# Performance work log

Measured on AMD Instinct MI355X. Metric: run time of the kernel, lower is better.

The kernel has to match this reference:

```python
import jax, jax.numpy as jnp
import numpy as np

N, E, B = 50000, 600000, 64
C_IN, H, C_OUT, L = 128, 128, 64, 3
BN_EPS = 1e-5


def setup_inputs() -> dict:
    key = jax.random.key(0)
    ks = iter(jax.random.split(key, 40))

    def w(shape, fan_in):
        return jax.random.normal(next(ks), shape, jnp.float32) / np.sqrt(fan_in).astype(np.float32)

    return {
        "x": jax.random.normal(next(ks), (N, C_IN), jnp.float32),
        "edge_index": jax.random.randint(next(ks), (2, E), 0, N),
        "batch": jnp.sort(jax.random.randint(next(ks), (N,), 0, B)),
        # GINConv MLPs: Linear(in,h) -> BN -> ReLU -> Linear(h,h)   (stacked over L; C_IN == H)
        "convW1": w((L, C_IN, H), C_IN), "convb1": jnp.zeros((L, H), jnp.float32),
        "bn_g": jnp.ones((L, H), jnp.float32), "bn_b": jnp.zeros((L, H), jnp.float32),
        "convW2": w((L, H, H), H), "convb2": jnp.zeros((L, H), jnp.float32),
        # reconstruction head: Linear(h,h)-ReLU-Linear(h,h)-ReLU-Linear(h,4)-ReLU
        "recW1": w((H, H), H), "recb1": jnp.zeros((H,), jnp.float32),
        "recW2": w((H, H), H), "recb2": jnp.zeros((H,), jnp.float32),
        "recW3": w((H, 4), H), "recb3": jnp.zeros((4,), jnp.float32),
        # final MLP([h,h,out], norm=None): Linear(h,h)-ReLU-(dropout, eval=identity)-Linear(h,out)
        "mlpW1": w((H, H), H), "mlpb1": jnp.zeros((H,), jnp.float32),
        "mlpW2": w((H, C_OUT), H), "mlpb2": jnp.zeros((C_OUT,), jnp.float32),
    }


def reference(x, edge_index, batch, convW1, convb1, bn_g, bn_b, convW2, convb2,
              recW1, recb1, recW2, recb2, recW3, recb3, mlpW1, mlpb1, mlpW2, mlpb2):
    src, dst = edge_index[0], edge_index[1]
    for l in range(L):
        # GIN aggregation: out_i = nn((1+eps)*x_i + sum_{j->i} x_j), eps = 0
        agg = jax.ops.segment_sum(x[src], dst, num_segments=N)  # [N, d]
        h = (x + agg) @ convW1[l] + convb1[l]                   # [N, H]
        mu = h.mean(axis=0)
        var = jnp.var(h, axis=0)                                # biased, torch BN train mode
        h = bn_g[l] * (h - mu) * jax.lax.rsqrt(var + BN_EPS) + bn_b[l]
        h = jax.nn.relu(h) @ convW2[l] + convb2[l]
        x = jax.nn.relu(h)                                      # outer .relu() in forward
    # reconstruction branch on node features
    x_rec = jax.nn.relu(x @ recW1 + recb1)
    x_rec = jax.nn.relu(x_rec @ recW2 + recb2)
    x_rec = jax.nn.relu(x_rec @ recW3 + recb3)                  # [N, 4]
    # global_add_pool keyed by graph id
    pooled = jax.ops.segment_sum(x, batch, num_segments=B)      # [B, H]
    out = jax.nn.relu(pooled @ mlpW1 + mlpb1) @ mlpW2 + mlpb2   # [B, C_OUT]
    return (out, x_rec)
```

## Files before the change

### kernel.cpp

```cpp
#include <hip/hip_runtime.h>

#define NN 50000
#define EE 600000
#define BB 64
#define CH 128
#define LL 3
#define NGB 391
#define NSB 196
#define NPB 392

typedef unsigned short u16;
typedef unsigned int u32;
typedef short s16x8 __attribute__((ext_vector_type(8)));
typedef float f32x4 __attribute__((ext_vector_type(4)));

__device__ __forceinline__ u16 f2b(float f) {
    u32 x = __float_as_uint(f);
    return (u16)((x + 0x7FFFu + ((x >> 16) & 1u)) >> 16);
}
__device__ __forceinline__ float b2f(u16 u) {
    return __uint_as_float(((u32)u) << 16);
}

__global__ __launch_bounds__(256) void k_zero2(int* __restrict__ deg,
                                               float* __restrict__ pooled,
                                               float* __restrict__ gstats) {
    int i = blockIdx.x * 256 + threadIdx.x;
    if (i < NN) deg[i] = 0;
    int j = i - NN;
    if (j >= 0 && j < BB * CH) pooled[j] = 0.f;
    int k = j - BB * CH;
    if (k >= 0 && k < 3 * 256) gstats[k] = 0.f;
}

__global__ __launch_bounds__(256) void k_count(const int* __restrict__ ei,
                                               int* __restrict__ deg) {
    int e = blockIdx.x * 256 + threadIdx.x;
    if (e < EE) atomicAdd(&deg[ei[EE + e]], 1);
}

__global__ __launch_bounds__(256) void k_scanA(const int* __restrict__ deg,
                                               int* __restrict__ bsum) {
    __shared__ int sm[256];
    int i = blockIdx.x * 256 + threadIdx.x;
    sm[threadIdx.x] = (i < NN) ? deg[i] : 0;
    __syncthreads();
    for (int off = 128; off > 0; off >>= 1) {
        if (threadIdx.x < off) sm[threadIdx.x] += sm[threadIdx.x + off];
        __syncthreads();
    }
    if (threadIdx.x == 0) bsum[blockIdx.x] = sm[0];
}

__global__ __launch_bounds__(256) void k_scanB(const int* __restrict__ deg,
                                               const int* __restrict__ bsum,
                                               int* __restrict__ rowptr,
                                               int* __restrict__ cur) {
    __shared__ int sb[256], sd[256];
    int t = threadIdx.x;
    sb[t] = (t < NSB) ? bsum[t] : 0;
    __syncthreads();
    for (int off = 1; off < 256; off <<= 1) {
        int v = (t >= off) ? sb[t - off] : 0;
        __syncthreads();
        sb[t] += v;
        __syncthreads();
    }
    int blockOff = (blockIdx.x == 0) ? 0 : sb[blockIdx.x - 1];
    int i = blockIdx.x * 256 + t;
    int d = (i < NN) ? deg[i] : 0;
    sd[t] = d;
    __syncthreads();
    for (int off = 1; off < 256; off <<= 1) {
        int v = (t >= off) ? sd[t - off] : 0;
        __syncthreads();
        sd[t] += v;
        __syncthreads();
    }
    int excl = blockOff + sd[t] - d;
    if (i < NN) { rowptr[i] = excl; cur[i] = excl; }
    if (i == NN - 1) rowptr[NN] = excl + d;
}

__global__ __launch_bounds__(256) void k_fill(const int* __restrict__ ei,
                                              int* __restrict__ cur,
                                              int* __restrict__ perm) {
    int e = blockIdx.x * 256 + threadIdx.x;
    if (e < EE) {
        int dst = ei[EE + e];
        int idx = atomicAdd(&cur[dst], 1);
        perm[idx] = ei[e];
    }
}

__global__ __launch_bounds__(256) void k_cvt(const float* __restrict__ x,
                                             u16* __restrict__ y) {
    long base = (long)(blockIdx.x * 256 + threadIdx.x) * 8;
    if (base < (long)NN * CH) {
        float4 f0 = *(const float4*)(x + base);
        float4 f1 = *(const float4*)(x + base + 4);
        union { u16 pk[8]; uint4 v; } uu;
        uu.pk[0] = f2b(f0.x); uu.pk[1] = f2b(f0.y);
        uu.pk[2] = f2b(f0.z); uu.pk[3] = f2b(f0.w);
        uu.pk[4] = f2b(f1.x); uu.pk[5] = f2b(f1.y);
        uu.pk[6] = f2b(f1.z); uu.pk[7] = f2b(f1.w);
        *(uint4*)(y + base) = uu.v;
    }
}

__global__ __launch_bounds__(256) void k_gather(const u16* __restrict__ x,
                                                const int* __restrict__ rowptr,
                                                const int* __restrict__ perm,
                                                u16* __restrict__ y) {
    int dst = blockIdx.x * 16 + (threadIdx.x >> 4);
    if (dst >= NN) return;
    int lane = threadIdx.x & 15;
    int co = lane * 8;
    int beg = rowptr[dst], end = rowptr[dst + 1];
    union { u16 pk[8]; uint4 v; } uu;
    uu.v = *(const uint4*)(x + (long)dst * CH + co);
    float a[8], b[8];
#pragma unroll
    for (int j = 0; j < 8; ++j) { a[j] = b2f(uu.pk[j]); b[j] = 0.f; }
    int e = beg;
    for (; e + 1 < end; e += 2) {
        int s0 = perm[e], s1 = perm[e + 1];
        union { u16 pk[8]; uint4 v; } v0, v1;
        v0.v = *(const uint4*)(x + (long)s0 * CH + co);
        v1.v = *(const uint4*)(x + (long)s1 * CH + co);
#pragma unroll
        for (int j = 0; j < 8; ++j) { a[j] += b2f(v0.pk[j]); b[j] += b2f(v1.pk[j]); }
    }
    if (e < end) {
        int s0 = perm[e];
        union { u16 pk[8]; uint4 v; } v0;
        v0.v = *(const uint4*)(x + (long)s0 * CH + co);
#pragma unroll
        for (int j = 0; j < 8; ++j) a[j] += b2f(v0.pk[j]);
    }
    union { u16 pk[8]; uint4 v; } ov;
#pragma unroll
    for (int j = 0; j < 8; ++j) ov.pk[j] = f2b(a[j] + b[j]);
    *(uint4*)(y + (long)dst * CH + co) = ov.v;
}

__global__ __launch_bounds__(256) void k_transpose_all(
    const float* __restrict__ cW1, const float* __restrict__ cW2,
    const float* __restrict__ rW1, const float* __restrict__ rW2,
    const float* __restrict__ rW3, u16* __restrict__ Wt) {
    int idx = blockIdx.x * 256 + threadIdx.x;
    if (idx < 8 * 16384) {
        int slot = idx >> 14;
        int wi = idx & 16383;
        int k = wi >> 7, n = wi & 127;
        const float* src = slot < 3 ? cW1 + slot * 16384
                         : slot < 6 ? cW2 + (slot - 3) * 16384
                         : slot == 6 ? rW1 : rW2;
        Wt[slot * 16384 + n * 128 + k] = f2b(src[wi]);
    } else if (idx < 9 * 16384) {
        int j = idx - 8 * 16384;
        int n = j >> 7, k = j & 127;
        Wt[8 * 16384 + j] = (n < 4) ? f2b(rW3[k * 4 + n]) : (u16)0;
    }
}

__device__ __forceinline__ void stageB8(const u16* __restrict__ Wt, u16* sB,
                                        int s, int rr) {
#pragma unroll
    for (int it = 0; it < 8; ++it) {
        int n = it * 16 + rr;
        uint4 u = *(const uint4*)(Wt + n * CH + 8 * s);
        *(uint4*)(&sB[n * CH + ((s ^ (n & 15)) * 8)]) = u;
    }
}

__device__ __forceinline__ void mfma8(const u16* sA, const u16* sB,
                                      f32x4 acc[2][8], int wv, int quad, int l16) {
    f32x4 z = {0.f, 0.f, 0.f, 0.f};
#pragma unroll
    for (int m = 0; m < 2; ++m)
#pragma unroll
        for (int t = 0; t < 8; ++t) acc[m][t] = z;
    const u16* pa0 = sA + (wv * 32 + l16) * CH;
    const u16* pa1 = pa0 + 16 * CH;
#pragma unroll
    for (int kc = 0; kc < 4; ++kc) {
        int off = (((kc << 2) | quad) ^ l16) << 3;
        s16x8 a0 = *(const s16x8*)(pa0 + off);
        s16x8 a1 = *(const s16x8*)(pa1 + off);
#pragma unroll
        for (int t = 0; t < 8; ++t) {
            s16x8 bfr = *(const s16x8*)(sB + (t * 16 + l16) * CH + off);
            acc[0][t] = __builtin_amdgcn_mfma_f32_16x16x32_bf16(a0, bfr, acc[0][t], 0, 0, 0);
            acc[1][t] = __builtin_amdgcn_mfma_f32_16x16x32_bf16(a1, bfr, acc[1][t], 0, 0, 0);
        }
    }
}

__device__ __forceinline__ void biasrelu(f32x4 acc[2][8],
                                         const float* __restrict__ bias, int l16) {
#pragma unroll
    for (int t = 0; t < 8; ++t) {
        float bv = bias[t * 16 + l16];
#pragma unroll
        for (int m = 0; m < 2; ++m)
#pragma unroll
            for (int r = 0; r < 4; ++r)
                acc[m][t][r] = fmaxf(acc[m][t][r] + bv, 0.f);
    }
}

__device__ __forceinline__ void restage(const f32x4 acc[2][8], u16* sA,
                                        int wv, int quad, int l16) {
#pragma unroll
    for (int t = 0; t < 8; ++t) {
        int chunk = (t << 1) | (l16 >> 3);
        int o7 = l16 & 7;
#pragma unroll
        for (int m = 0; m < 2; ++m)
#pragma unroll
            for (int r = 0; r < 4; ++r) {
                int lr = wv * 32 + m * 16 + quad * 4 + r;
                sA[lr * CH + ((chunk ^ (lr & 15)) << 3) + o7] = f2b(acc[m][t][r]);
            }
    }
}

__global__ __launch_bounds__(256, 2) void k_gemm1(
    u16* __restrict__ hy, const u16* __restrict__ Wt, int layer,
    const float* __restrict__ cb1, float* __restrict__ gstats) {
    __shared__ u16 sA[128 * CH];
    __shared__ u16 sB[128 * CH];
    const int tid = threadIdx.x;
    const int s = tid & 15, rr = tid >> 4;
    const int r0 = blockIdx.x * 128;
    const int lane = tid & 63, wv = tid >> 6, quad = lane >> 4, l16 = lane & 15;

    stageB8(Wt + layer * 16384, sB, s, rr);
#pragma unroll
    for (int it = 0; it < 8; ++it) {
        int lr = it * 16 + rr, gr = r0 + lr;
        union { u16 pk[8]; uint4 v; } uu;
        if (gr < NN) {
            uu.v = *(const uint4*)(hy + (long)gr * CH + 8 * s);
        } else {
#pragma unroll
            for (int j = 0; j < 8; ++j) uu.pk[j] = 0;
        }
        *(uint4*)(&sA[lr * CH + ((s ^ (lr & 15)) * 8)]) = uu.v;
    }
    __syncthreads();
    f32x4 acc[2][8];
    mfma8(sA, sB, acc, wv, quad, l16);

    float ss[8], qq[8];
#pragma unroll
    for (int t = 0; t < 8; ++t) {
        float bv = cb1[t * 16 + l16];
        ss[t] = 0.f; qq[t] = 0.f;
#pragma unroll
        for (int m = 0; m < 2; ++m) {
            int rbase = r0 + wv * 32 + m * 16 + quad * 4;
#pragma unroll
            for (int r = 0; r < 4; ++r) {
                float v = acc[m][t][r] + bv;
                acc[m][t][r] = v;
                if (rbase + r < NN) { ss[t] += v; qq[t] += v * v; }
            }
        }
    }
#pragma unroll
    for (int t = 0; t < 8; ++t) {
        ss[t] += __shfl_xor(ss[t], 16);
        ss[t] += __shfl_xor(ss[t], 32);
        qq[t] += __shfl_xor(qq[t], 16);
        qq[t] += __shfl_xor(qq[t], 32);
    }
    float* red = (float*)sA;
    __syncthreads();
    if (lane < 16) {
#pragma unroll
        for (int t = 0; t < 8; ++t) {
            red[wv * 256 + t * 16 + l16] = ss[t];
            red[wv * 256 + 128 + t * 16 + l16] = qq[t];
        }
    }
    __syncthreads();
    unsafeAtomicAdd(&gstats[tid],
                    red[tid] + red[256 + tid] + red[512 + tid] + red[768 + tid]);

#pragma unroll
    for (int t = 0; t < 8; ++t) {
        int col = t * 16 + l16;
#pragma unroll
        for (int m = 0; m < 2; ++m)
#pragma unroll
            for (int r = 0; r < 4; ++r) {
                int row = r0 + wv * 32 + m * 16 + quad * 4 + r;
                if (row < NN) hy[(long)row * CH + col] = f2b(acc[m][t][r]);
            }
    }
}

template <bool LAST>
__global__ __launch_bounds__(256, 2) void k_gemm2(
    const u16* __restrict__ h16, const u16* __restrict__ Wt, int layer,
    const float* __restrict__ g, const float* __restrict__ bbeta,
    const float* __restrict__ gstats, const float* __restrict__ cb2,
    u16* __restrict__ xc,
    const float* __restrict__ rb1, const float* __restrict__ rb2,
    const float* __restrict__ rb3, float* __restrict__ x_rec) {
    __shared__ u16 sA[128 * CH];
    __shared__ u16 sB[128 * CH];
    __shared__ float snorm[256];
    const int tid = threadIdx.x;
    const int s = tid & 15, rr = tid >> 4;
    const int r0 = blockIdx.x * 128;
    const int lane = tid & 63, wv = tid >> 6, quad = lane >> 4, l16 = lane & 15;

    if (tid < 128) {
        float sum = gstats[tid];
        float sq = gstats[128 + tid];
        float mu = sum / (float)NN;
        float var = sq / (float)NN - mu * mu;
        float sc = g[tid] * rsqrtf(var + 1e-5f);
        snorm[tid] = sc;
        snorm[128 + tid] = bbeta[tid] - mu * sc;
    }
    stageB8(Wt + (3 + layer) * 16384, sB, s, rr);
    __syncthreads();

#pragma unroll
    for (int it = 0; it < 8; ++it) {
        int lr = it * 16 + rr, gr = r0 + lr;
        union { u16 pk[8]; uint4 v; } uu;
        if (gr < NN) {
            uu.v = *(const uint4*)(h16 + (long)gr * CH + 8 * s);
#pragma unroll
            for (int j = 0; j < 8; ++j) {
                int c = 8 * s + j;
                float v = fmaxf(b2f(uu.pk[j]) * snorm[c] + snorm[128 + c], 0.f);
                uu.pk[j] = f2b(v);
            }
        } else {
#pragma unroll
            for (int j = 0; j < 8; ++j) uu.pk[j] = 0;
        }
        *(uint4*)(&sA[lr * CH + ((s ^ (lr & 15)) * 8)]) = uu.v;
    }
    __syncthreads();
    f32x4 acc[2][8];
    mfma8(sA, sB, acc, wv, quad, l16);
    biasrelu(acc, cb2, l16);
#pragma unroll
    for (int t = 0; t < 8; ++t) {
        int col = t * 16 + l16;
#pragma unroll
        for (int m = 0; m < 2; ++m)
#pragma unroll
            for (int r = 0; r < 4; ++r) {
                int row = r0 + wv * 32 + m * 16 + quad * 4 + r;
                if (row < NN) xc[(long)row * CH + col] = f2b(acc[m][t][r]);
            }
    }

    if constexpr (LAST) {
        __syncthreads();
        restage(acc, sA, wv, quad, l16);
        stageB8(Wt + 6 * 16384, sB, s, rr);
        __syncthreads();
        mfma8(sA, sB, acc, wv, quad, l16);
        biasrelu(acc, rb1, l16);
        __syncthreads();
        restage(acc, sA, wv, quad, l16);
        stageB8(Wt + 7 * 16384, sB, s, rr);
        __syncthreads();
        mfma8(sA, sB, acc, wv, quad, l16);
        biasrelu(acc, rb2, l16);
        __syncthreads();
        restage(acc, sA, wv, quad, l16);
        {
            int n = rr;
            uint4 u = *(const uint4*)(Wt + 8 * 16384 + n * CH + 8 * s);
            *(uint4*)(&sB[n * CH + ((s ^ (n & 15)) * 8)]) = u;
        }
        __syncthreads();
        f32x4 a4[2];
        a4[0] = (f32x4){0.f, 0.f, 0.f, 0.f};
        a4[1] = (f32x4){0.f, 0.f, 0.f, 0.f};
        const u16* pa0 = sA + (wv * 32 + l16) * CH;
        const u16* pa1 = pa0 + 16 * CH;
#pragma unroll
        for (int kc = 0; kc < 4; ++kc) {
            int off = (((kc << 2) | quad) ^ l16) << 3;
            s16x8 a0 = *(const s16x8*)(pa0 + off);
            s16x8 a1 = *(const s16x8*)(pa1 + off);
            s16x8 bfr = *(const s16x8*)(sB + l16 * CH + off);
            a4[0] = __builtin_amdgcn_mfma_f32_16x16x32_bf16(a0, bfr, a4[0], 0, 0, 0);
            a4[1] = __builtin_amdgcn_mfma_f32_16x16x32_bf16(a1, bfr, a4[1], 0, 0, 0);
        }
        if (l16 < 4) {
            float bv = rb3[l16];
#pragma unroll
            for (int m = 0; m < 2; ++m)
#pragma unroll
                for (int r = 0; r < 4; ++r) {
                    int row = r0 + wv * 32 + m * 16 + quad * 4 + r;
                    if (row < NN) x_rec[(long)row * 4 + l16] = fmaxf(a4[m][r] + bv, 0.f);
                }
        }
    }
}

__global__ __launch_bounds__(256) void k_pool(const u16* __restrict__ x,
                                              const int* __restrict__ batch,
                                              float* __restrict__ pooled) {
    int r0 = blockIdx.x * 128;
    if (r0 >= NN) return;
    int rend = r0 + 128 < NN ? r0 + 128 : NN;
    int c = threadIdx.x & 127;
    int half = threadIdx.x >> 7;
    int r = r0 + half;
    if (r >= rend) return;
    int g = batch[r];
    float s = 0.f;
    for (; r < rend; r += 2) {
        int gg = batch[r];
        if (gg != g) {
            unsafeAtomicAdd(pooled + g * CH + c, s);
            s = 0.f;
            g = gg;
        }
        s += b2f(x[(long)r * CH + c]);
    }
    unsafeAtomicAdd(pooled + g * CH + c, s);
}

__global__ __launch_bounds__(128) void k_mlp(const float* __restrict__ pooled,
                                             const float* __restrict__ W1,
                                             const float* __restrict__ b1,
                                             const float* __restrict__ W2,
                                             const float* __restrict__ b2,
                                             float* __restrict__ out) {
    __shared__ float p[128], t1[128];
    int b = blockIdx.x, t = threadIdx.x;
    p[t] = pooled[b * CH + t];
    __syncthreads();
    float acc = b1[t];
    for (int k = 0; k < 128; ++k) acc += p[k] * W1[k * 128 + t];
    t1[t] = fmaxf(acc, 0.f);
    __syncthreads();
    if (t < 64) {
        float o = b2[t];
        for (int k = 0; k < 128; ++k) o += t1[k] * W2[k * 64 + t];
        out[b * 64 + t] = o;
    }
}

extern "C" void kernel_launch(void* const* d_in, const int* in_sizes, int n_in,
                              void* d_out, int out_size, void* d_ws, size_t ws_size,
                              hipStream_t stream) {
    const float* x_in   = (const float*)d_in[0];
    const int*   ei     = (const int*)d_in[1];
    const int*   batch  = (const int*)d_in[2];
    const float* convW1 = (const float*)d_in[3];
    const float* convb1 = (const float*)d_in[4];
    const float* bn_g   = (const float*)d_in[5];
    const float* bn_b   = (const float*)d_in[6];
    const float* convW2 = (const float*)d_in[7];
    const float* convb2 = (const float*)d_in[8];
    const float* recW1  = (const float*)d_in[9];
    const float* recb1  = (const float*)d_in[10];
    const float* recW2  = (const float*)d_in[11];
    const float* recb2  = (const float*)d_in[12];
    const float* recW3  = (const float*)d_in[13];
    const float* recb3  = (const float*)d_in[14];
    const float* mlpW1  = (const float*)d_in[15];
    const float* mlpb1  = (const float*)d_in[16];
    const float* mlpW2  = (const float*)d_in[17];
    const float* mlpb2  = (const float*)d_in[18];

    float* out   = (float*)d_out;
    float* x_rec = out + 4096;

    char* w = (char*)d_ws;
    u16*   x16    = (u16*)w;    w += (size_t)NN * CH * 2;
    u16*   y16    = (u16*)w;    w += (size_t)NN * CH * 2;
    u16*   xc     = (u16*)w;    w += (size_t)NN * CH * 2;
    u16*   Wt     = (u16*)w;    w += (size_t)9 * 16384 * 2;
    float* gstats = (float*)w;  w += (size_t)3 * 256 * 4;
    float* pooled = (float*)w;  w += (size_t)BB * CH * 4;
    int*   deg    = (int*)w;    w += (size_t)NN * 4;
    int*   bsum   = (int*)w;    w += (size_t)NSB * 4;
    int*   rowptr = (int*)w;    w += (size_t)(NN + 1) * 4;
    int*   cur    = (int*)w;    w += (size_t)NN * 4;
    int*   perm   = (int*)w;    w += (size_t)EE * 4;

    dim3 b256(256), b128(128);

    k_zero2<<<231, b256, 0, stream>>>(deg, pooled, gstats);
    k_count<<<2344, b256, 0, stream>>>(ei, deg);
    k_scanA<<<NSB, b256, 0, stream>>>(deg, bsum);
    k_scanB<<<NSB, b256, 0, stream>>>(deg, bsum, rowptr, cur);
    k_fill<<<2344, b256, 0, stream>>>(ei, cur, perm);
    k_cvt<<<3125, b256, 0, stream>>>(x_in, x16);
    k_transpose_all<<<576, b256, 0, stream>>>(convW1, convW2, recW1, recW2, recW3, Wt);

    const u16* cur_x = x16;
    for (int l = 0; l < LL; ++l) {
        k_gather<<<3125, b256, 0, stream>>>(cur_x, rowptr, perm, y16);
        k_gemm1<<<NGB, b256, 0, stream>>>(y16, Wt, l, convb1 + l * 128,
                                          gstats + l * 256);
        if (l < LL - 1)
            k_gemm2<false><<<NGB, b256, 0, stream>>>(
                y16, Wt, l, bn_g + l * 128, bn_b + l * 128, gstats + l * 256,
                convb2 + l * 128, xc, recb1, recb2, recb3, x_rec);
        else
            k_gemm2<true><<<NGB, b256, 0, stream>>>(
                y16, Wt, l, bn_g + l * 128, bn_b + l * 128, gstats + l * 256,
                convb2 + l * 128, xc, recb1, recb2, recb3, x_rec);
        cur_x = xc;
    }
    k_pool<<<NPB, b256, 0, stream>>>(xc, batch, pooled);
    k_mlp<<<64, b128, 0, stream>>>(pooled, mlpW1, mlpb1, mlpW2, mlpb2, out);
}
```

Before: 383.0 us.

## Fuse neighbor gather into first GEMM, shrink row tile, merge prep kernels

The CSR neighbor aggregation moves into the first GEMM kernel, so each block builds its A tile in shared memory straight from gathered rows and never writes or re-reads an intermediate aggregate buffer. The row tile drops from 128 to 64, which doubles the block count and raises occupancy to 3 blocks per CU. The conversion, weight transpose and zeroing kernels are merged into one prep launch. In exchange, the GEMM blocks now carry the irregular gather latency, and each block restages the weight tile to serve half as many rows.

```diff
diff --git a/kernel.cpp b/kernel.cpp
--- a/kernel.cpp
+++ b/kernel.cpp
@@ -5,7 +5,8 @@
 #define BB 64
 #define CH 128
 #define LL 3
-#define NGB 391
+#define TR 64
+#define NGB 782
 #define NSB 196
 #define NPB 392
 
@@ -22,15 +23,44 @@
     return __uint_as_float(((u32)u) << 16);
 }
 
-__global__ __launch_bounds__(256) void k_zero2(int* __restrict__ deg,
-                                               float* __restrict__ pooled,
-                                               float* __restrict__ gstats) {
-    int i = blockIdx.x * 256 + threadIdx.x;
-    if (i < NN) deg[i] = 0;
-    int j = i - NN;
-    if (j >= 0 && j < BB * CH) pooled[j] = 0.f;
-    int k = j - BB * CH;
-    if (k >= 0 && k < 3 * 256) gstats[k] = 0.f;
+__global__ __launch_bounds__(256) void k_prep(
+    const float* __restrict__ x, u16* __restrict__ x16,
+    const float* __restrict__ cW1, const float* __restrict__ cW2,
+    const float* __restrict__ rW1, const float* __restrict__ rW2,
+    const float* __restrict__ rW3, u16* __restrict__ Wt,
+    int* __restrict__ deg, float* __restrict__ pooled,
+    float* __restrict__ gstats) {
+    int gid = blockIdx.x * 256 + threadIdx.x;
+
+    long base = (long)gid * 8;
+    if (base < (long)NN * CH) {
+        float4 f0 = *(const float4*)(x + base);
+        float4 f1 = *(const float4*)(x + base + 4);
+        union { u16 pk[8]; uint4 v; } uu;
+        uu.pk[0] = f2b(f0.x); uu.pk[1] = f2b(f0.y);
+        uu.pk[2] = f2b(f0.z); uu.pk[3] = f2b(f0.w);
+        uu.pk[4] = f2b(f1.x); uu.pk[5] = f2b(f1.y);
+        uu.pk[6] = f2b(f1.z); uu.pk[7] = f2b(f1.w);
+        *(uint4*)(x16 + base) = uu.v;
+    }
+    if (gid < 8 * 16384) {
+        int slot = gid >> 14;
+        int wi = gid & 16383;
+        int k = wi >> 7, n = wi & 127;
+        const float* src = slot < 3 ? cW1 + slot * 16384
+                         : slot < 6 ? cW2 + (slot - 3) * 16384
+                         : slot == 6 ? rW1 : rW2;
+        Wt[slot * 16384 + n * 128 + k] = f2b(src[wi]);
+    } else if (gid < 9 * 16384) {
+        int j = gid - 8 * 16384;
+        int n = j >> 7, k = j & 127;
+        Wt[8 * 16384 + j] = (n < 4) ? f2b(rW3[k * 4 + n]) : (u16)0;
+    }
+    if (gid < NN) deg[gid] = 0;
+    int j2 = gid - NN;
+    if (j2 >= 0 && j2 < BB * CH) pooled[j2] = 0.f;
+    int k2 = j2 - BB * CH;
+    if (k2 >= 0 && k2 < 3 * 256) gstats[k2] = 0.f;
 }
 
 __global__ __launch_bounds__(256) void k_count(const int* __restrict__ ei,
@@ -93,77 +123,6 @@
     }
 }
 
-__global__ __launch_bounds__(256) void k_cvt(const float* __restrict__ x,
-                                             u16* __restrict__ y) {
-    long base = (long)(blockIdx.x * 256 + threadIdx.x) * 8;
-    if (base < (long)NN * CH) {
-        float4 f0 = *(const float4*)(x + base);
-        float4 f1 = *(const float4*)(x + base + 4);
-        union { u16 pk[8]; uint4 v; } uu;
-        uu.pk[0] = f2b(f0.x); uu.pk[1] = f2b(f0.y);
-        uu.pk[2] = f2b(f0.z); uu.pk[3] = f2b(f0.w);
-        uu.pk[4] = f2b(f1.x); uu.pk[5] = f2b(f1.y);
-        uu.pk[6] = f2b(f1.z); uu.pk[7] = f2b(f1.w);
-        *(uint4*)(y + base) = uu.v;
-    }
-}
-
-__global__ __launch_bounds__(256) void k_gather(const u16* __restrict__ x,
-                                                const int* __restrict__ rowptr,
-                                                const int* __restrict__ perm,
-                                                u16* __restrict__ y) {
-    int dst = blockIdx.x * 16 + (threadIdx.x >> 4);
-    if (dst >= NN) return;
-    int lane = threadIdx.x & 15;
-    int co = lane * 8;
-    int beg = rowptr[dst], end = rowptr[dst + 1];
-    union { u16 pk[8]; uint4 v; } uu;
-    uu.v = *(const uint4*)(x + (long)dst * CH + co);
-    float a[8], b[8];
-#pragma unroll
-    for (int j = 0; j < 8; ++j) { a[j] = b2f(uu.pk[j]); b[j] = 0.f; }
-    int e = beg;
-    for (; e + 1 < end; e += 2) {
-        int s0 = perm[e], s1 = perm[e + 1];
-        union { u16 pk[8]; uint4 v; } v0, v1;
-        v0.v = *(const uint4*)(x + (long)s0 * CH + co);
-        v1.v = *(const uint4*)(x + (long)s1 * CH + co);
-#pragma unroll
-        for (int j = 0; j < 8; ++j) { a[j] += b2f(v0.pk[j]); b[j] += b2f(v1.pk[j]); }
-    }
-    if (e < end) {
-        int s0 = perm[e];
-        union { u16 pk[8]; uint4 v; } v0;
-        v0.v = *(const uint4*)(x + (long)s0 * CH + co);
-#pragma unroll
-        for (int j = 0; j < 8; ++j) a[j] += b2f(v0.pk[j]);
-    }
-    union { u16 pk[8]; uint4 v; } ov;
-#pragma unroll
-    for (int j = 0; j < 8; ++j) ov.pk[j] = f2b(a[j] + b[j]);
-    *(uint4*)(y + (long)dst * CH + co) = ov.v;
-}
-
-__global__ __launch_bounds__(256) void k_transpose_all(
-    const float* __restrict__ cW1, const float* __restrict__ cW2,
-    const float* __restrict__ rW1, const float* __restrict__ rW2,
-    const float* __restrict__ rW3, u16* __restrict__ Wt) {
-    int idx = blockIdx.x * 256 + threadIdx.x;
-    if (idx < 8 * 16384) {
-        int slot = idx >> 14;
-        int wi = idx & 16383;
-        int k = wi >> 7, n = wi & 127;
-        const float* src = slot < 3 ? cW1 + slot * 16384
-                         : slot < 6 ? cW2 + (slot - 3) * 16384
-                         : slot == 6 ? rW1 : rW2;
-        Wt[slot * 16384 + n * 128 + k] = f2b(src[wi]);
-    } else if (idx < 9 * 16384) {
-        int j = idx - 8 * 16384;
-        int n = j >> 7, k = j & 127;
-        Wt[8 * 16384 + j] = (n < 4) ? f2b(rW3[k * 4 + n]) : (u16)0;
-    }
-}
-
 __device__ __forceinline__ void stageB8(const u16* __restrict__ Wt, u16* sB,
                                         int s, int rr) {
 #pragma unroll
@@ -174,99 +133,130 @@
     }
 }
 
-__device__ __forceinline__ void mfma8(const u16* sA, const u16* sB,
-                                      f32x4 acc[2][8], int wv, int quad, int l16) {
+template <int M>
+__device__ __forceinline__ void mfmaT(const u16* sA, const u16* sB,
+                                      f32x4 (&acc)[M][8], int rowbase, int quad,
+                                      int l16) {
     f32x4 z = {0.f, 0.f, 0.f, 0.f};
 #pragma unroll
-    for (int m = 0; m < 2; ++m)
+    for (int m = 0; m < M; ++m)
 #pragma unroll
         for (int t = 0; t < 8; ++t) acc[m][t] = z;
-    const u16* pa0 = sA + (wv * 32 + l16) * CH;
-    const u16* pa1 = pa0 + 16 * CH;
 #pragma unroll
     for (int kc = 0; kc < 4; ++kc) {
         int off = (((kc << 2) | quad) ^ l16) << 3;
-        s16x8 a0 = *(const s16x8*)(pa0 + off);
-        s16x8 a1 = *(const s16x8*)(pa1 + off);
+        s16x8 a[M];
+#pragma unroll
+        for (int m = 0; m < M; ++m)
+            a[m] = *(const s16x8*)(sA + (rowbase + m * 16 + l16) * CH + off);
 #pragma unroll
         for (int t = 0; t < 8; ++t) {
             s16x8 bfr = *(const s16x8*)(sB + (t * 16 + l16) * CH + off);
-            acc[0][t] = __builtin_amdgcn_mfma_f32_16x16x32_bf16(a0, bfr, acc[0][t], 0, 0, 0);
-            acc[1][t] = __builtin_amdgcn_mfma_f32_16x16x32_bf16(a1, bfr, acc[1][t], 0, 0, 0);
-        }
-    }
-}
-
-__device__ __forceinline__ void biasrelu(f32x4 acc[2][8],
-                                         const float* __restrict__ bias, int l16) {
+#pragma unroll
+            for (int m = 0; m < M; ++m)
+                acc[m][t] = __builtin_amdgcn_mfma_f32_16x16x32_bf16(a[m], bfr, acc[m][t], 0, 0, 0);
+        }
+    }
+}
+
+template <int M>
+__device__ __forceinline__ void biasreluT(f32x4 (&acc)[M][8],
+                                          const float* __restrict__ bias, int l16) {
 #pragma unroll
     for (int t = 0; t < 8; ++t) {
         float bv = bias[t * 16 + l16];
 #pragma unroll
-        for (int m = 0; m < 2; ++m)
+        for (int m = 0; m < M; ++m)
 #pragma unroll
             for (int r = 0; r < 4; ++r)
                 acc[m][t][r] = fmaxf(acc[m][t][r] + bv, 0.f);
     }
 }
 
-__device__ __forceinline__ void restage(const f32x4 acc[2][8], u16* sA,
-                                        int wv, int quad, int l16) {
+template <int M>
+__device__ __forceinline__ void restageT(const f32x4 (&acc)[M][8], u16* sA,
+                                         int rowbase, int quad, int l16) {
 #pragma unroll
     for (int t = 0; t < 8; ++t) {
         int chunk = (t << 1) | (l16 >> 3);
         int o7 = l16 & 7;
 #pragma unroll
-        for (int m = 0; m < 2; ++m)
+        for (int m = 0; m < M; ++m)
 #pragma unroll
             for (int r = 0; r < 4; ++r) {
-                int lr = wv * 32 + m * 16 + quad * 4 + r;
+                int lr = rowbase + m * 16 + quad * 4 + r;
                 sA[lr * CH + ((chunk ^ (lr & 15)) << 3) + o7] = f2b(acc[m][t][r]);
             }
     }
 }
 
-__global__ __launch_bounds__(256, 2) void k_gemm1(
-    u16* __restrict__ hy, const u16* __restrict__ Wt, int layer,
-    const float* __restrict__ cb1, float* __restrict__ gstats) {
-    __shared__ u16 sA[128 * CH];
+__global__ __launch_bounds__(256, 3) void k_gg1(
+    const u16* __restrict__ x, const int* __restrict__ rowptr,
+    const int* __restrict__ perm, const u16* __restrict__ Wt, int layer,
+    const float* __restrict__ cb1, float* __restrict__ gstats,
+    u16* __restrict__ h16) {
+    __shared__ u16 sA[TR * CH];
     __shared__ u16 sB[128 * CH];
     const int tid = threadIdx.x;
     const int s = tid & 15, rr = tid >> 4;
-    const int r0 = blockIdx.x * 128;
+    const int r0 = blockIdx.x * TR;
     const int lane = tid & 63, wv = tid >> 6, quad = lane >> 4, l16 = lane & 15;
 
     stageB8(Wt + layer * 16384, sB, s, rr);
-#pragma unroll
-    for (int it = 0; it < 8; ++it) {
-        int lr = it * 16 + rr, gr = r0 + lr;
-        union { u16 pk[8]; uint4 v; } uu;
-        if (gr < NN) {
-            uu.v = *(const uint4*)(hy + (long)gr * CH + 8 * s);
-        } else {
-#pragma unroll
-            for (int j = 0; j < 8; ++j) uu.pk[j] = 0;
-        }
-        *(uint4*)(&sA[lr * CH + ((s ^ (lr & 15)) * 8)]) = uu.v;
-    }
-    __syncthreads();
-    f32x4 acc[2][8];
-    mfma8(sA, sB, acc, wv, quad, l16);
+
+    {
+        int co = s * 8;
+#pragma unroll
+        for (int rl = rr; rl < TR; rl += 16) {
+            int dst = r0 + rl;
+            float a[8], b[8];
+#pragma unroll
+            for (int j = 0; j < 8; ++j) { a[j] = 0.f; b[j] = 0.f; }
+            if (dst < NN) {
+                union { u16 pk[8]; uint4 v; } uu;
+                uu.v = *(const uint4*)(x + (long)dst * CH + co);
+#pragma unroll
+                for (int j = 0; j < 8; ++j) a[j] = b2f(uu.pk[j]);
+                int beg = rowptr[dst], end = rowptr[dst + 1];
+                int e = beg;
+                for (; e + 1 < end; e += 2) {
+                    int s0 = perm[e], s1 = perm[e + 1];
+                    union { u16 pk[8]; uint4 v; } v0, v1;
+                    v0.v = *(const uint4*)(x + (long)s0 * CH + co);
+                    v1.v = *(const uint4*)(x + (long)s1 * CH + co);
+#pragma unroll
+                    for (int j = 0; j < 8; ++j) { a[j] += b2f(v0.pk[j]); b[j] += b2f(v1.pk[j]); }
+                }
+                if (e < end) {
+                    int s0 = perm[e];
+                    union { u16 pk[8]; uint4 v; } v0;
+                    v0.v = *(const uint4*)(x + (long)s0 * CH + co);
+#pragma unroll
+                    for (int j = 0; j < 8; ++j) a[j] += b2f(v0.pk[j]);
+                }
+            }
+            union { u16 pk[8]; uint4 v; } ov;
+#pragma unroll
+            for (int j = 0; j < 8; ++j) ov.pk[j] = f2b(a[j] + b[j]);
+            *(uint4*)(&sA[rl * CH + ((s ^ (rl & 15)) * 8)]) = ov.v;
+        }
+    }
+    __syncthreads();
+
+    f32x4 acc[1][8];
+    mfmaT<1>(sA, sB, acc, wv * 16, quad, l16);
 
     float ss[8], qq[8];
 #pragma unroll
     for (int t = 0; t < 8; ++t) {
         float bv = cb1[t * 16 + l16];
         ss[t] = 0.f; qq[t] = 0.f;
-#pragma unroll
-        for (int m = 0; m < 2; ++m) {
-            int rbase = r0 + wv * 32 + m * 16 + quad * 4;
-#pragma unroll
-            for (int r = 0; r < 4; ++r) {
-                float v = acc[m][t][r] + bv;
-                acc[m][t][r] = v;
-                if (rbase + r < NN) { ss[t] += v; qq[t] += v * v; }
-            }
+        int rbase = r0 + wv * 16 + quad * 4;
+#pragma unroll
+        for (int r = 0; r < 4; ++r) {
+            float v = acc[0][t][r] + bv;
+            acc[0][t][r] = v;
+            if (rbase + r < NN) { ss[t] += v; qq[t] += v * v; }
         }
     }
 #pragma unroll
@@ -276,6 +266,17 @@
         qq[t] += __shfl_xor(qq[t], 16);
         qq[t] += __shfl_xor(qq[t], 32);
     }
+
+#pragma unroll
+    for (int t = 0; t < 8; ++t) {
+        int col = t * 16 + l16;
+#pragma unroll
+        for (int r = 0; r < 4; ++r) {
+            int row = r0 + wv * 16 + quad * 4 + r;
+            if (row < NN) h16[(long)row * CH + col] = f2b(acc[0][t][r]);
+        }
+    }
+
     float* red = (float*)sA;
     __syncthreads();
     if (lane < 16) {
@@ -288,34 +289,22 @@
     __syncthreads();
     unsafeAtomicAdd(&gstats[tid],
                     red[tid] + red[256 + tid] + red[512 + tid] + red[768 + tid]);
-
-#pragma unroll
-    for (int t = 0; t < 8; ++t) {
-        int col = t * 16 + l16;
-#pragma unroll
-        for (int m = 0; m < 2; ++m)
-#pragma unroll
-            for (int r = 0; r < 4; ++r) {
-                int row = r0 + wv * 32 + m * 16 + quad * 4 + r;
-                if (row < NN) hy[(long)row * CH + col] = f2b(acc[m][t][r]);
-            }
-    }
 }
 
 template <bool LAST>
-__global__ __launch_bounds__(256, 2) void k_gemm2(
+__global__ __launch_bounds__(256, 3) void k_gemm2(
     const u16* __restrict__ h16, const u16* __restrict__ Wt, int layer,
     const float* __restrict__ g, const float* __restrict__ bbeta,
     const float* __restrict__ gstats, const float* __restrict__ cb2,
     u16* __restrict__ xc,
     const float* __restrict__ rb1, const float* __restrict__ rb2,
     const float* __restrict__ rb3, float* __restrict__ x_rec) {
-    __shared__ u16 sA[128 * CH];
+    __shared__ u16 sA[TR * CH];
     __shared__ u16 sB[128 * CH];
     __shared__ float snorm[256];
     const int tid = threadIdx.x;
     const int s = tid & 15, rr = tid >> 4;
-    const int r0 = blockIdx.x * 128;
+    const int r0 = blockIdx.x * TR;
     const int lane = tid & 63, wv = tid >> 6, quad = lane >> 4, l16 = lane & 15;
 
     if (tid < 128) {
@@ -331,7 +320,7 @@
     __syncthreads();
 
 #pragma unroll
-    for (int it = 0; it < 8; ++it) {
+    for (int it = 0; it < 4; ++it) {
         int lr = it * 16 + rr, gr = r0 + lr;
         union { u16 pk[8]; uint4 v; } uu;
         if (gr < NN) {
@@ -349,65 +338,56 @@
         *(uint4*)(&sA[lr * CH + ((s ^ (lr & 15)) * 8)]) = uu.v;
     }
     __syncthreads();
-    f32x4 acc[2][8];
-    mfma8(sA, sB, acc, wv, quad, l16);
-    biasrelu(acc, cb2, l16);
+    f32x4 acc[1][8];
+    mfmaT<1>(sA, sB, acc, wv * 16, quad, l16);
+    biasreluT<1>(acc, cb2, l16);
 #pragma unroll
     for (int t = 0; t < 8; ++t) {
         int col = t * 16 + l16;
 #pragma unroll
-        for (int m = 0; m < 2; ++m)
-#pragma unroll
-            for (int r = 0; r < 4; ++r) {
-                int row = r0 + wv * 32 + m * 16 + quad * 4 + r;
-                if (row < NN) xc[(long)row * CH + col] = f2b(acc[m][t][r]);
-            }
+        for (int r = 0; r < 4; ++r) {
+            int row = r0 + wv * 16 + quad * 4 + r;
+            if (row < NN) xc[(long)row * CH + col] = f2b(acc[0][t][r]);
+        }
     }
 
     if constexpr (LAST) {
         __syncthreads();
-        restage(acc, sA, wv, quad, l16);
+        restageT<1>(acc, sA, wv * 16, quad, l16);
         stageB8(Wt + 6 * 16384, sB, s, rr);
         __syncthreads();
-        mfma8(sA, sB, acc, wv, quad, l16);
-        biasrelu(acc, rb1, l16);
-        __syncthreads();
-        restage(acc, sA, wv, quad, l16);
+        mfmaT<1>(sA, sB, acc, wv * 16, quad, l16);
+        biasreluT<1>(acc, rb1, l16);
+        __syncthreads();
+        restageT<1>(acc, sA, wv * 16, quad, l16);
         stageB8(Wt + 7 * 16384, sB, s, rr);
         __syncthreads();
-        mfma8(sA, sB, acc, wv, quad, l16);
-        biasrelu(acc, rb2, l16);
-        __syncthreads();
-        restage(acc, sA, wv, quad, l16);
+        mfmaT<1>(sA, sB, acc, wv * 16, quad, l16);
+        biasreluT<1>(acc, rb2, l16);
+        __syncthreads();
+        restageT<1>(acc, sA, wv * 16, quad, l16);
         {
             int n = rr;
             uint4 u = *(const uint4*)(Wt + 8 * 16384 + n * CH + 8 * s);
             *(uint4*)(&sB[n * CH + ((s ^ (n & 15)) * 8)]) = u;
         }
         __syncthreads();
-        f32x4 a4[2];
-        a4[0] = (f32x4){0.f, 0.f, 0.f, 0.f};
-        a4[1] = (f32x4){0.f, 0.f, 0.f, 0.f};
-        const u16* pa0 = sA + (wv * 32 + l16) * CH;
-        const u16* pa1 = pa0 + 16 * CH;
+        f32x4 a4 = {0.f, 0.f, 0.f, 0.f};
+        const u16* pa0 = sA + (wv * 16 + l16) * CH;
 #pragma unroll
         for (int kc = 0; kc < 4; ++kc) {
             int off = (((kc << 2) | quad) ^ l16) << 3;
             s16x8 a0 = *(const s16x8*)(pa0 + off);
-            s16x8 a1 = *(const s16x8*)(pa1 + off);
             s16x8 bfr = *(const s16x8*)(sB + l16 * CH + off);
-            a4[0] = __builtin_amdgcn_mfma_f32_16x16x32_bf16(a0, bfr, a4[0], 0, 0, 0);
-            a4[1] = __builtin_amdgcn_mfma_f32_16x16x32_bf16(a1, bfr, a4[1], 0, 0, 0);
+            a4 = __builtin_amdgcn_mfma_f32_16x16x32_bf16(a0, bfr, a4, 0, 0, 0);
         }
         if (l16 < 4) {
             float bv = rb3[l16];
 #pragma unroll
-            for (int m = 0; m < 2; ++m)
-#pragma unroll
-                for (int r = 0; r < 4; ++r) {
-                    int row = r0 + wv * 32 + m * 16 + quad * 4 + r;
-                    if (row < NN) x_rec[(long)row * 4 + l16] = fmaxf(a4[m][r] + bv, 0.f);
-                }
+            for (int r = 0; r < 4; ++r) {
+                int row = r0 + wv * 16 + quad * 4 + r;
+                if (row < NN) x_rec[(long)row * 4 + l16] = fmaxf(a4[r] + bv, 0.f);
+            }
         }
     }
 }
@@ -485,7 +465,7 @@
 
     char* w = (char*)d_ws;
     u16*   x16    = (u16*)w;    w += (size_t)NN * CH * 2;
-    u16*   y16    = (u16*)w;    w += (size_t)NN * CH * 2;
+    u16*   h16    = (u16*)w;    w += (size_t)NN * CH * 2;
     u16*   xc     = (u16*)w;    w += (size_t)NN * CH * 2;
     u16*   Wt     = (u16*)w;    w += (size_t)9 * 16384 * 2;
     float* gstats = (float*)w;  w += (size_t)3 * 256 * 4;
@@ -498,26 +478,24 @@
 
     dim3 b256(256), b128(128);
 
-    k_zero2<<<231, b256, 0, stream>>>(deg, pooled, gstats);
+    k_prep<<<3125, b256, 0, stream>>>(x_in, x16, convW1, convW2, recW1, recW2,
+                                      recW3, Wt, deg, pooled, gstats);
     k_count<<<2344, b256, 0, stream>>>(ei, deg);
     k_scanA<<<NSB, b256, 0, stream>>>(deg, bsum);
     k_scanB<<<NSB, b256, 0, stream>>>(deg, bsum, rowptr, cur);
     k_fill<<<2344, b256, 0, stream>>>(ei, cur, perm);
-    k_cvt<<<3125, b256, 0, stream>>>(x_in, x16);
-    k_transpose_all<<<576, b256, 0, stream>>>(convW1, convW2, recW1, recW2, recW3, Wt);
 
     const u16* cur_x = x16;
     for (int l = 0; l < LL; ++l) {
-        k_gather<<<3125, b256, 0, stream>>>(cur_x, rowptr, perm, y16);
-        k_gemm1<<<NGB, b256, 0, stream>>>(y16, Wt, l, convb1 + l * 128,
-                                          gstats + l * 256);
+        k_gg1<<<NGB, b256, 0, stream>>>(cur_x, rowptr, perm, Wt, l,
+                                        convb1 + l * 128, gstats + l * 256, h16);
         if (l < LL - 1)
             k_gemm2<false><<<NGB, b256, 0, stream>>>(
-                y16, Wt, l, bn_g + l * 128, bn_b + l * 128, gstats + l * 256,
+                h16, Wt, l, bn_g + l * 128, bn_b + l * 128, gstats + l * 256,
                 convb2 + l * 128, xc, recb1, recb2, recb3, x_rec);
         else
             k_gemm2<true><<<NGB, b256, 0, stream>>>(
-                y16, Wt, l, bn_g + l * 128, bn_b + l * 128, gstats + l * 256,
+                h16, Wt, l, bn_g + l * 128, bn_b + l * 128, gstats + l * 256,
                 convb2 + l * 128, xc, recb1, recb2, recb3, x_rec);
         cur_x = xc;
     }
```

New measurement: 476.2 us. 24.3% more time.
